# Kernel tuning notes

Hardware: AMD Instinct MI355X
Metric: run time of the kernel (lower is better)

The kernel has to match this reference:

```python
import jax, jax.numpy as jnp
import numpy as np

B, T, N, H = 4096, 128, 128, 128  # batch, timesteps, input_size, encoder_num_hidden
EPS = 1e-5  # BatchNorm1d eps


def setup_inputs() -> dict:
    key = jax.random.key(0)
    ks = jax.random.split(key, 12)
    g = lambda k, shp, s=0.088: jax.random.normal(k, shp, dtype=jnp.float32) * s  # ~1/sqrt(H)
    return {
        "X": jax.random.normal(ks[0], (B, T, N), dtype=jnp.float32),
        "attn_w": g(ks[1], (2 * H + T,)),
        "attn_b": jnp.zeros((), jnp.float32),
        "bn_gamma": jnp.ones((N,), jnp.float32),
        "bn_beta": jnp.zeros((N,), jnp.float32),
        "W_ih0": g(ks[2], (4 * H, N)),
        "W_hh0": g(ks[3], (4 * H, H)),
        "b_ih0": g(ks[4], (4 * H,)),
        "b_hh0": g(ks[5], (4 * H,)),
        "W_ih1": g(ks[6], (4 * H, H)),
        "W_hh1": g(ks[7], (4 * H, H)),
        "b_ih1": g(ks[8], (4 * H,)),
        "b_hh1": g(ks[9], (4 * H,)),
    }


def _lstm_cell(x, h, c, W_ih, W_hh, b):
    # torch gate order: i, f, g, o
    gates = x @ W_ih.T + h @ W_hh.T + b  # (B, 4H)
    i, f, gg, o = jnp.split(gates, 4, axis=-1)
    c_new = jax.nn.sigmoid(f) * c + jax.nn.sigmoid(i) * jnp.tanh(gg)
    h_new = jax.nn.sigmoid(o) * jnp.tanh(c_new)
    return h_new, c_new


def reference(X, attn_w, attn_b, bn_gamma, bn_beta,
              W_ih0, W_hh0, b_ih0, b_hh0, W_ih1, W_hh1, b_ih1, b_hh1):
    # Attention input per step is cat(h_top repeat, s_top repeat, X^T) -> Linear(2H+T -> 1).
    # The X^T contribution is time-invariant; precompute it once.
    w_h, w_s, w_x = attn_w[:H], attn_w[H:2 * H], attn_w[2 * H:]
    Xp = jnp.transpose(X, (0, 2, 1))            # (B, N, T) driving-series view
    score_x = Xp @ w_x + attn_b                 # (B, N)
    b0 = b_ih0 + b_hh0
    b1 = b_ih1 + b_hh1

    def step(carry, x_t):
        h0, c0, h1, c1 = carry                  # layer0/layer1 hidden & cell (B, H)
        # h_n[-1], s_n[-1] are broadcast identically over all N features
        scores = score_x + (h1 @ w_h)[:, None] + (c1 @ w_s)[:, None]  # (B, N)
        alpha = jax.nn.softmax(scores, axis=1)
        x_tilde = alpha * x_t                   # (B, N)
        # BatchNorm1d in training mode: batch statistics over dim 0
        mean = jnp.mean(x_tilde, axis=0)
        var = jnp.var(x_tilde, axis=0)
        xb = (x_tilde - mean) * jax.lax.rsqrt(var + EPS) * bn_gamma + bn_beta
        # 2-layer LSTM single step (dropout inactive in eval)
        h0n, c0n = _lstm_cell(xb, h0, c0, W_ih0, W_hh0, b0)
        h1n, c1n = _lstm_cell(h0n, h1, c1, W_ih1, W_hh1, b1)
        return (h0n, c0n, h1n, c1n), (x_tilde, h1n)

    zeros = jnp.zeros((B, H), X.dtype)
    init = (zeros, zeros, zeros, zeros)
    Xt = jnp.transpose(X, (1, 0, 2))            # (T, B, N) for scan
    _, (xt_seq, he_seq) = jax.lax.scan(step, init, Xt)
    X_tilde = jnp.transpose(xt_seq, (1, 0, 2))   # (B, T, N)
    X_encoded = jnp.transpose(he_seq, (1, 0, 2)) # (B, T, H)
    return X_tilde, X_encoded
```

## Files before the change

### kernel.cpp

```cpp
#include <hip/hip_runtime.h>
#include <cstdint>
#include <cstddef>

#define B_ 4096
#define T_ 128
#define N_ 128
#define H_ 128
#define G4_ 512
#define KC_ 256
#define EPS_ 1e-5f

#define RPB_ 16
#define NB_ 256
#define W0K_ 128
#define W0P_ 136

#define KB_ 512
#define ROWS_ 8
#define PSBLK_ 16384

typedef _Float16 f16x8 __attribute__((ext_vector_type(8)));
typedef _Float16 f16x4 __attribute__((ext_vector_type(4)));
typedef float f32x4 __attribute__((ext_vector_type(4)));

__device__ __forceinline__ float sigm_(float x) { return 1.f / (1.f + __expf(-x)); }
__device__ __forceinline__ float tanh_(float x) {
  float ax = fabsf(x);
  float e = __expf(-2.f * ax);
  float t = (1.f - e) / (1.f + e);
  return copysignf(t, x);
}

__global__ void k0_prep(const float* __restrict__ Wih0, const float* __restrict__ Whh0,
                        const float* __restrict__ bih0, const float* __restrict__ bhh0,
                        const float* __restrict__ Wih1, const float* __restrict__ Whh1,
                        const float* __restrict__ bih1, const float* __restrict__ bhh1,
                        _Float16* __restrict__ Wpack, float* __restrict__ bpack) {
  int idx = blockIdx.x * blockDim.x + threadIdx.x;
  if (idx < 2 * G4_ * KC_) {
    int k = idx & (KC_ - 1);
    int j = (idx >> 8) & (G4_ - 1);
    int l = idx >> 17;
    const float* Wih = l ? Wih1 : Wih0;
    const float* Whh = l ? Whh1 : Whh0;
    float v = (k < N_) ? Wih[j * N_ + k] : Whh[j * N_ + (k - N_)];
    Wpack[idx] = (_Float16)v;
  }
  if (idx < 2 * G4_) {
    int j = idx & (G4_ - 1);
    bpack[idx] = (idx >> 9) ? (bih1[j] + bhh1[j]) : (bih0[j] + bhh0[j]);
  }
}

__global__ __launch_bounds__(256, 2) void k12_fused(
    const float* __restrict__ X, const float* __restrict__ attn_w,
    const float* __restrict__ attn_b, float* __restrict__ out0,
    float* __restrict__ psum, float* __restrict__ psq) {
  __shared__ float xs[T_ * N_];
  __shared__ float wx[T_];
  __shared__ float redS[2][N_];
  __shared__ float redM[4], redE[4];
  const int tid = threadIdx.x;
  const int blk = blockIdx.x;
  const int n = tid & 127;
  const int th = tid >> 7;
  const int wv = tid >> 6;
  if (tid < T_) wx[tid] = attn_w[2 * H_ + tid];
  const float ab = attn_b[0];
  float sum[64], sq[64];
#pragma unroll
  for (int i = 0; i < 64; ++i) { sum[i] = 0.f; sq[i] = 0.f; }

  for (int rb = 0; rb < ROWS_; ++rb) {
    const int b = blk * ROWS_ + rb;
    const float* xb = X + (size_t)b * T_ * N_;
    __syncthreads();
#pragma unroll
    for (int i = 0; i < 16; ++i) {
      int fi = ((i << 8) + tid) << 2;
      *(f32x4*)&xs[fi] = *(const f32x4*)&xb[fi];
    }
    __syncthreads();
    float s = 0.f;
#pragma unroll 8
    for (int tt = 0; tt < 64; ++tt) {
      int t = (th << 6) + tt;
      s = fmaf(xs[t * N_ + n], wx[t], s);
    }
    redS[th][n] = s;
    __syncthreads();
    s = redS[0][n] + redS[1][n] + ab;
    float m = s;
#pragma unroll
    for (int off = 32; off >= 1; off >>= 1) m = fmaxf(m, __shfl_xor(m, off));
    if ((tid & 63) == 0) redM[wv] = m;
    __syncthreads();
    m = fmaxf(fmaxf(redM[0], redM[1]), fmaxf(redM[2], redM[3]));
    float e = __expf(s - m);
    float sm = e;
#pragma unroll
    for (int off = 32; off >= 1; off >>= 1) sm += __shfl_xor(sm, off);
    if ((tid & 63) == 0) redE[wv] = sm;
    __syncthreads();
    sm = redE[0] + redE[1];
    const float alpha = e / sm;
    const size_t obase = ((size_t)b * T_ + (th << 6)) * N_ + n;
#pragma unroll
    for (int tt = 0; tt < 64; ++tt) {
      float v = alpha * xs[((th << 6) + tt) * N_ + n];
      sum[tt] += v;
      sq[tt] += v * v;
      out0[obase + (size_t)tt * N_] = v;
    }
  }
  float* pbs = psum + (size_t)blk * PSBLK_ + th * 8192 + n;
  float* pbq = psq + (size_t)blk * PSBLK_ + th * 8192 + n;
#pragma unroll
  for (int tt = 0; tt < 64; ++tt) {
    pbs[tt * 128] = sum[tt];
    pbq[tt * 128] = sq[tt];
  }
}

__global__ void k3r(const float* __restrict__ psum, const float* __restrict__ psq,
                    const float* __restrict__ gamma, const float* __restrict__ beta,
                    float* __restrict__ scale, float* __restrict__ shift) {
  const int t = blockIdx.x;
  const int n = threadIdx.x;
  const int th = t >> 6, tt = t & 63;
  const size_t off = (size_t)th * 8192 + tt * 128 + n;
  float s = 0.f, q = 0.f;
  for (int blk = 0; blk < KB_; ++blk) {
    s += psum[(size_t)blk * PSBLK_ + off];
    q += psq[(size_t)blk * PSBLK_ + off];
  }
  float mean = s * (1.f / B_);
  float var = q * (1.f / B_) - mean * mean;
  float rstd = rsqrtf(var + EPS_);
  float g = gamma[n];
  scale[t * N_ + n] = rstd * g;
  shift[t * N_ + n] = beta[n] - mean * rstd * g;
}

__global__ __launch_bounds__(512, 2) void k4_recur(
    const float* __restrict__ xt , const _Float16* __restrict__ Wpack,
    const float* __restrict__ bpack, const float* __restrict__ scale,
    const float* __restrict__ shift, float* __restrict__ out1) {
  __shared__ _Float16 W0l[G4_][W0P_];
  __shared__ _Float16 A0[RPB_][264];
  __shared__ _Float16 A1[RPB_][264];

  const int tid = threadIdx.x;
  const int w = tid >> 6;
  const int lane = tid & 63;
  const int quad = lane >> 4;
  const int l16 = lane & 15;
  const int nb = blockIdx.x;
  const int col = (w << 4) + l16;

  {
    const _Float16* src = Wpack + (size_t)tid * KC_;
#pragma unroll
    for (int kk = 0; kk < W0K_; kk += 8)
      *(f16x8*)&W0l[tid][kk] = *(const f16x8*)&src[kk];
  }

  f16x8 w1[4][8];
#pragma unroll
  for (int g = 0; g < 4; ++g) {
    const _Float16* src = Wpack + (size_t)(G4_ + (g << 7) + col) * KC_ + (quad << 3);
#pragma unroll
    for (int kb = 0; kb < 8; ++kb) w1[g][kb] = *(const f16x8*)&src[kb << 5];
  }

  float bia0[4], bia1[4];
#pragma unroll
  for (int g = 0; g < 4; ++g) {
    bia0[g] = bpack[(g << 7) + col];
    bia1[g] = bpack[G4_ + (g << 7) + col];
  }

  float c0[4], c1[4];
#pragma unroll
  for (int e = 0; e < 4; ++e) { c0[e] = 0.f; c1[e] = 0.f; }

  const int sr = tid >> 5;
  const int sc = (tid & 31) << 2;
  const size_t browbase = (size_t)(nb * RPB_ + sr) * T_;

  {
    f32x4 xv = *(const f32x4*)(xt + (browbase + 0) * N_ + sc);
    f32x4 s4 = *(const f32x4*)(scale + sc);
    f32x4 h4 = *(const f32x4*)(shift + sc);
    f16x4 hv;
#pragma unroll
    for (int e = 0; e < 4; ++e) hv[e] = (_Float16)fmaf(xv[e], s4[e], h4[e]);
    *(f16x4*)&A0[sr][sc] = hv;
    f16x4 z = {};
    *(f16x4*)&A0[sr][N_ + sc] = z;
    *(f16x4*)&A1[sr][N_ + sc] = z;
  }
  __syncthreads();

  for (int t = 0; t < T_; ++t) {
    f32x4 xn = {};
    if (t + 1 < T_) xn = *(const f32x4*)(xt + (browbase + t + 1) * N_ + sc);

    f32x4 acc[4] = {};
#pragma unroll
    for (int kb = 0; kb < 8; ++kb) {
      f16x8 a = *(const f16x8*)&A0[l16][(kb << 5) + (quad << 3)];
      if (kb < 4) {
#pragma unroll
        for (int g = 0; g < 4; ++g) {
          f16x8 bf = *(const f16x8*)&W0l[(g << 7) + col][(kb << 5) + (quad << 3)];
          acc[g] = __builtin_amdgcn_mfma_f32_16x16x32_f16(a, bf, acc[g], 0, 0, 0);
        }
      } else {
#pragma unroll
        for (int g = 0; g < 4; ++g) {
          f16x8 bf = *(const f16x8*)(Wpack + (size_t)((g << 7) + col) * KC_ +
                                     (kb << 5) + (quad << 3));
          acc[g] = __builtin_amdgcn_mfma_f32_16x16x32_f16(a, bf, acc[g], 0, 0, 0);
        }
      }
    }

    _Float16 h0h[4];
#pragma unroll
    for (int e = 0; e < 4; ++e) {
      float ig = acc[0][e] + bia0[0];
      float fg = acc[1][e] + bia0[1];
      float gg = acc[2][e] + bia0[2];
      float og = acc[3][e] + bia0[3];
      float cn = sigm_(fg) * c0[e] + sigm_(ig) * tanh_(gg);
      c0[e] = cn;
      h0h[e] = (_Float16)(sigm_(og) * tanh_(cn));
    }
    __syncthreads();
#pragma unroll
    for (int e = 0; e < 4; ++e) {
      A0[(quad << 2) + e][N_ + col] = h0h[e];
      A1[(quad << 2) + e][col] = h0h[e];
    }
    __syncthreads();

    f16x8 a1[8];
#pragma unroll
    for (int kb = 0; kb < 4; ++kb) {
      a1[kb] = *(const f16x8*)&A1[l16][(kb << 5) + (quad << 3)];
      a1[4 + kb] = *(const f16x8*)&A1[l16][128 + (kb << 5) + (quad << 3)];
    }
    f32x4 acc1[4] = {};
#pragma unroll
    for (int kb = 0; kb < 8; ++kb) {
#pragma unroll
      for (int g = 0; g < 4; ++g)
        acc1[g] = __builtin_amdgcn_mfma_f32_16x16x32_f16(a1[kb], w1[g][kb], acc1[g], 0, 0, 0);
    }

    _Float16 h1h[4];
#pragma unroll
    for (int e = 0; e < 4; ++e) {
      float ig = acc1[0][e] + bia1[0];
      float fg = acc1[1][e] + bia1[1];
      float gg = acc1[2][e] + bia1[2];
      float og = acc1[3][e] + bia1[3];
      float cn = sigm_(fg) * c1[e] + sigm_(ig) * tanh_(gg);
      c1[e] = cn;
      float hn = sigm_(og) * tanh_(cn);
      h1h[e] = (_Float16)hn;
      out1[((size_t)(nb * RPB_ + (quad << 2) + e) * T_ + t) * H_ + col] = hn;
    }
    __syncthreads();
#pragma unroll
    for (int e = 0; e < 4; ++e)
      A1[(quad << 2) + e][N_ + col] = h1h[e];
    if (t + 1 < T_) {
      f32x4 s4 = *(const f32x4*)(scale + (t + 1) * N_ + sc);
      f32x4 h4 = *(const f32x4*)(shift + (t + 1) * N_ + sc);
      f16x4 hv;
#pragma unroll
      for (int e = 0; e < 4; ++e) hv[e] = (_Float16)fmaf(xn[e], s4[e], h4[e]);
      *(f16x4*)&A0[sr][sc] = hv;
    }
    __syncthreads();
  }
}

extern "C" void kernel_launch(void* const* d_in, const int* in_sizes, int n_in,
                              void* d_out, int out_size, void* d_ws, size_t ws_size,
                              hipStream_t stream) {
  const float* X = (const float*)d_in[0];
  const float* attnw = (const float*)d_in[1];
  const float* attnb = (const float*)d_in[2];
  const float* gamma = (const float*)d_in[3];
  const float* beta = (const float*)d_in[4];
  const float* Wih0 = (const float*)d_in[5];
  const float* Whh0 = (const float*)d_in[6];
  const float* bih0 = (const float*)d_in[7];
  const float* bhh0 = (const float*)d_in[8];
  const float* Wih1 = (const float*)d_in[9];
  const float* Whh1 = (const float*)d_in[10];
  const float* bih1 = (const float*)d_in[11];
  const float* bhh1 = (const float*)d_in[12];

  float* out0 = (float*)d_out;
  float* out1 = out0 + (size_t)B_ * T_ * N_;

  float* psum = out1;
  float* psq = out1 + (size_t)KB_ * PSBLK_;

  float* ws = (float*)d_ws;
  float* scale = ws;
  float* shift = scale + T_ * N_;
  float* bpack = shift + T_ * N_;
  _Float16* Wpack = (_Float16*)(bpack + 2 * G4_);

  k0_prep<<<1024, 256, 0, stream>>>(Wih0, Whh0, bih0, bhh0, Wih1, Whh1, bih1, bhh1,
                                    Wpack, bpack);
  k12_fused<<<KB_, 256, 0, stream>>>(X, attnw, attnb, out0, psum, psq);
  k3r<<<T_, N_, 0, stream>>>(psum, psq, gamma, beta, scale, shift);
  k4_recur<<<NB_, 512, 0, stream>>>(out0, Wpack, bpack, scale, shift, out1);
}
```

Baseline: 1.385 ms.

## Double-buffer X rows in attention/BN-stats kernel and widen stats reduction

The attention and BatchNorm-statistics kernel now runs 256 blocks of 512 threads, each handling 16 batch rows. The next row is prefetched from global memory into registers and then stored into a second LDS buffer while the current row is processed. Each thread covers 32 timesteps instead of 64, and the number of partial-sum slabs is halved. The stats reduction kernel uses 256 threads that split the slab loop in two and combine through shared memory. The aim is to hide global load latency and cut partial-sum traffic, at the cost of lower occupancy (one large block per CU) and twice the LDS footprint.

```diff
diff --git a/kernel.cpp b/kernel.cpp
--- a/kernel.cpp
+++ b/kernel.cpp
@@ -15,9 +15,8 @@
 #define W0K_ 128
 #define W0P_ 136
 
-#define KB_ 512
-#define ROWS_ 8
-#define PSBLK_ 16384
+#define KB2_ 256
+#define ROWS2_ 16
 
 typedef _Float16 f16x8 __attribute__((ext_vector_type(8)));
 typedef _Float16 f16x4 __attribute__((ext_vector_type(4)));
@@ -52,50 +51,66 @@
   }
 }
 
-__global__ __launch_bounds__(256, 2) void k12_fused(
+__global__ __launch_bounds__(512, 1) void k12_fused(
     const float* __restrict__ X, const float* __restrict__ attn_w,
     const float* __restrict__ attn_b, float* __restrict__ out0,
     float* __restrict__ psum, float* __restrict__ psq) {
-  __shared__ float xs[T_ * N_];
+  __shared__ float xs[2 * T_ * N_];
   __shared__ float wx[T_];
-  __shared__ float redS[2][N_];
-  __shared__ float redM[4], redE[4];
+  __shared__ float redS[4][N_];
+  __shared__ float redM[8], redE[8];
   const int tid = threadIdx.x;
   const int blk = blockIdx.x;
   const int n = tid & 127;
-  const int th = tid >> 7;
+  const int tq = tid >> 7;
   const int wv = tid >> 6;
+  const int row0 = blk * ROWS2_;
   if (tid < T_) wx[tid] = attn_w[2 * H_ + tid];
   const float ab = attn_b[0];
-  float sum[64], sq[64];
-#pragma unroll
-  for (int i = 0; i < 64; ++i) { sum[i] = 0.f; sq[i] = 0.f; }
-
-  for (int rb = 0; rb < ROWS_; ++rb) {
-    const int b = blk * ROWS_ + rb;
-    const float* xb = X + (size_t)b * T_ * N_;
-    __syncthreads();
-#pragma unroll
-    for (int i = 0; i < 16; ++i) {
-      int fi = ((i << 8) + tid) << 2;
+
+  float sum[32], sq[32];
+#pragma unroll
+  for (int i = 0; i < 32; ++i) { sum[i] = 0.f; sq[i] = 0.f; }
+
+  {
+    const float* xb = X + (size_t)row0 * T_ * N_;
+#pragma unroll
+    for (int i = 0; i < 8; ++i) {
+      int fi = ((i << 9) + tid) << 2;
       *(f32x4*)&xs[fi] = *(const f32x4*)&xb[fi];
     }
-    __syncthreads();
+  }
+
+  int buf = 0;
+  for (int rb = 0; rb < ROWS2_; ++rb) {
+    __syncthreads();
+    const float* xcur = xs + (buf << 14);
+
+    f32x4 stg[8];
+    if (rb + 1 < ROWS2_) {
+      const float* xb1 = X + (size_t)(row0 + rb + 1) * T_ * N_;
+#pragma unroll
+      for (int i = 0; i < 8; ++i)
+        stg[i] = *(const f32x4*)&xb1[((i << 9) + tid) << 2];
+    }
+
     float s = 0.f;
-#pragma unroll 8
-    for (int tt = 0; tt < 64; ++tt) {
-      int t = (th << 6) + tt;
-      s = fmaf(xs[t * N_ + n], wx[t], s);
-    }
-    redS[th][n] = s;
-    __syncthreads();
-    s = redS[0][n] + redS[1][n] + ab;
+#pragma unroll
+    for (int tt = 0; tt < 32; ++tt) {
+      int t = (tq << 5) + tt;
+      s = fmaf(xcur[t * N_ + n], wx[t], s);
+    }
+    redS[tq][n] = s;
+    __syncthreads();
+    s = redS[0][n] + redS[1][n] + redS[2][n] + redS[3][n] + ab;
+
     float m = s;
 #pragma unroll
     for (int off = 32; off >= 1; off >>= 1) m = fmaxf(m, __shfl_xor(m, off));
     if ((tid & 63) == 0) redM[wv] = m;
     __syncthreads();
-    m = fmaxf(fmaxf(redM[0], redM[1]), fmaxf(redM[2], redM[3]));
+    m = fmaxf(fmaxf(fmaxf(redM[0], redM[1]), fmaxf(redM[2], redM[3])),
+              fmaxf(fmaxf(redM[4], redM[5]), fmaxf(redM[6], redM[7])));
     float e = __expf(s - m);
     float sm = e;
 #pragma unroll
@@ -104,42 +119,64 @@
     __syncthreads();
     sm = redE[0] + redE[1];
     const float alpha = e / sm;
-    const size_t obase = ((size_t)b * T_ + (th << 6)) * N_ + n;
-#pragma unroll
-    for (int tt = 0; tt < 64; ++tt) {
-      float v = alpha * xs[((th << 6) + tt) * N_ + n];
+
+    if (rb + 1 < ROWS2_) {
+      float* xnx = xs + ((buf ^ 1) << 14);
+#pragma unroll
+      for (int i = 0; i < 8; ++i)
+        *(f32x4*)&xnx[((i << 9) + tid) << 2] = stg[i];
+    }
+
+    const size_t b = (size_t)(row0 + rb);
+#pragma unroll
+    for (int tt = 0; tt < 32; ++tt) {
+      int t = (tq << 5) + tt;
+      float v = alpha * xcur[t * N_ + n];
       sum[tt] += v;
       sq[tt] += v * v;
-      out0[obase + (size_t)tt * N_] = v;
-    }
-  }
-  float* pbs = psum + (size_t)blk * PSBLK_ + th * 8192 + n;
-  float* pbq = psq + (size_t)blk * PSBLK_ + th * 8192 + n;
-#pragma unroll
-  for (int tt = 0; tt < 64; ++tt) {
-    pbs[tt * 128] = sum[tt];
-    pbq[tt * 128] = sq[tt];
+      out0[(b * T_ + t) * N_ + n] = v;
+    }
+    buf ^= 1;
+  }
+
+  float* pbs = psum + ((size_t)blk << 14) + (tq << 5) * N_ + n;
+  float* pbq = psq + ((size_t)blk << 14) + (tq << 5) * N_ + n;
+#pragma unroll
+  for (int tt = 0; tt < 32; ++tt) {
+    pbs[tt * N_] = sum[tt];
+    pbq[tt * N_] = sq[tt];
   }
 }
 
 __global__ void k3r(const float* __restrict__ psum, const float* __restrict__ psq,
                     const float* __restrict__ gamma, const float* __restrict__ beta,
                     float* __restrict__ scale, float* __restrict__ shift) {
+  __shared__ float rs[2][N_], rq[2][N_];
   const int t = blockIdx.x;
-  const int n = threadIdx.x;
-  const int th = t >> 6, tt = t & 63;
-  const size_t off = (size_t)th * 8192 + tt * 128 + n;
+  const int tid = threadIdx.x;
+  const int n = tid & 127;
+  const int hb = tid >> 7;
+  const size_t off = (size_t)t * N_ + n;
   float s = 0.f, q = 0.f;
-  for (int blk = 0; blk < KB_; ++blk) {
-    s += psum[(size_t)blk * PSBLK_ + off];
-    q += psq[(size_t)blk * PSBLK_ + off];
-  }
-  float mean = s * (1.f / B_);
-  float var = q * (1.f / B_) - mean * mean;
-  float rstd = rsqrtf(var + EPS_);
-  float g = gamma[n];
-  scale[t * N_ + n] = rstd * g;
-  shift[t * N_ + n] = beta[n] - mean * rstd * g;
+#pragma unroll 4
+  for (int i = 0; i < 128; ++i) {
+    size_t o = ((size_t)((hb << 7) + i) << 14) + off;
+    s += psum[o];
+    q += psq[o];
+  }
+  rs[hb][n] = s;
+  rq[hb][n] = q;
+  __syncthreads();
+  if (hb == 0) {
+    s = rs[0][n] + rs[1][n];
+    q = rq[0][n] + rq[1][n];
+    float mean = s * (1.f / B_);
+    float var = q * (1.f / B_) - mean * mean;
+    float rstd = rsqrtf(var + EPS_);
+    float g = gamma[n];
+    scale[t * N_ + n] = rstd * g;
+    shift[t * N_ + n] = beta[n] - mean * rstd * g;
+  }
 }
 
 __global__ __launch_bounds__(512, 2) void k4_recur(
@@ -309,7 +346,7 @@
   float* out1 = out0 + (size_t)B_ * T_ * N_;
 
   float* psum = out1;
-  float* psq = out1 + (size_t)KB_ * PSBLK_;
+  float* psq = out1 + ((size_t)KB2_ << 14);
 
   float* ws = (float*)d_ws;
   float* scale = ws;
@@ -319,7 +356,7 @@
 
   k0_prep<<<1024, 256, 0, stream>>>(Wih0, Whh0, bih0, bhh0, Wih1, Whh1, bih1, bhh1,
                                     Wpack, bpack);
-  k12_fused<<<KB_, 256, 0, stream>>>(X, attnw, attnb, out0, psum, psq);
-  k3r<<<T_, N_, 0, stream>>>(psum, psq, gamma, beta, scale, shift);
+  k12_fused<<<KB2_, 512, 0, stream>>>(X, attnw, attnb, out0, psum, psq);
+  k3r<<<T_, 256, 0, stream>>>(psum, psq, gamma, beta, scale, shift);
   k4_recur<<<NB_, 512, 0, stream>>>(out0, Wpack, bpack, scale, shift, out1);
 }
```

Result: faster. 1.332 ms (-3.9%).
